# Optimization experiments

Measured on AMD Instinct MI355X. Metric: run time of the kernel, lower is better.

Reference implementation:

```python
import jax, jax.numpy as jnp
import numpy as np

N = 50000      # nodes
E = 800000     # unique directed edges (avg degree 16)
F = 64         # input_dim
D = 64         # output_dim (== F -> residual is identity)
ALPHA = 0.5
LCS_THR = 0.5  # enable_lcs_masking=True, lcs_threshold=0.5


def setup_inputs() -> dict:
    key = jax.random.key(0)
    ks = jax.random.split(key, 16)
    x = jax.random.normal(ks[0], (N, F), jnp.float32)
    src = jax.random.randint(ks[1], (E,), 0, N, jnp.int32)
    dst = jax.random.randint(ks[2], (E,), 0, N, jnp.int32)
    # integer-valued multiplicities in {1,2,3,4} (recurring-transaction counts)
    counts = jnp.floor(jax.random.uniform(ks[3], (E,), jnp.float32) * 4.0) + 1.0
    def lin(k, fan_in, shape):
        return jax.random.normal(k, shape, jnp.float32) / np.float32(np.sqrt(fan_in))
    return dict(
        x=x, counts=counts,
        W_s2d=lin(ks[4], F, (F, D)), b_s2d=jnp.zeros((D,), jnp.float32),
        W_d2s=lin(ks[5], F, (F, D)), b_d2s=jnp.zeros((D,), jnp.float32),
        W_l1=lin(ks[6], 2 * F, (2 * F, F)), b_l1=jnp.zeros((F,), jnp.float32),
        W_l2=lin(ks[7], F, (F, 1)), b_l2=jnp.zeros((1,), jnp.float32),
        W_g1=lin(ks[8], 2 * D, (2 * D, D)), b_g1=jnp.zeros((D,), jnp.float32),
        W_g2=lin(ks[9], D, (D, 1)), b_g2=jnp.zeros((1,), jnp.float32),
        src=src, dst=dst,
    )


def reference(x, counts, W_s2d, b_s2d, W_d2s, b_d2s,
              W_l1, b_l1, W_l2, b_l2, W_g1, b_g1, W_g2, b_g2,
              src, dst):
    # in/out degrees from full (unmasked) multiplicities, clamped at 1
    in_deg = jnp.maximum(jax.ops.segment_sum(counts, dst, num_segments=N), 1.0)
    out_deg = jnp.maximum(jax.ops.segment_sum(counts, src, num_segments=N), 1.0)

    # LCS per unique edge: sigmoid(MLP([x_src, x_dst])), detached in torch
    lcs_in = jnp.concatenate([x[src], x[dst]], axis=-1)          # [E, 2F]
    lcs = jax.nn.sigmoid(
        jax.nn.relu(lcs_in @ W_l1 + b_l1) @ W_l2 + b_l2)[:, 0]   # [E]
    lcs = jax.lax.stop_gradient(lcs)
    keep = (lcs >= LCS_THR).astype(x.dtype)                      # LCS masking

    # symmetric-normalized edge weights with multiplicity counts
    w = counts * keep * jax.lax.rsqrt(out_deg[src] * in_deg[dst])  # [E]

    # direction-aware message passing (redundancy-eliminated, per unique edge)
    h_s2d = x @ W_s2d + b_s2d                                    # [N, D]
    h_d2s = x @ W_d2s + b_d2s                                    # [N, D]
    m_in = jax.ops.segment_sum(w[:, None] * h_s2d[src], dst, num_segments=N)
    m_out = jax.ops.segment_sum(w[:, None] * h_d2s[dst], src, num_segments=N)

    # node-wise gating over inbound vs outbound flows
    gate = jax.nn.sigmoid(
        jax.nn.relu(jnp.concatenate([m_in, m_out], axis=-1) @ W_g1 + b_g1)
        @ W_g2 + b_g2)                                           # [N, 1]

    # gated alpha-blend + identity residual (input_dim == output_dim)
    out = ALPHA * gate * m_in + (1.0 - ALPHA) * (1.0 - gate) * m_out + x
    return out
```

## Files before the change

### kernel.cpp

```cpp
#include <hip/hip_runtime.h>
#include <math.h>


typedef unsigned long long u64;

#define SLOTS 56

__device__ __forceinline__ float bflo(unsigned u) { return __uint_as_float(u << 16); }
__device__ __forceinline__ float bfhi(unsigned u) { return __uint_as_float(u & 0xffff0000u); }
__device__ __forceinline__ unsigned rne16(float f) {
    unsigned u = __float_as_uint(f);
    return (u + 0x7fffu + ((u >> 16) & 1u)) >> 16;
}

__global__ __launch_bounds__(256) void proj_zero_kernel(
    const float* __restrict__ x,
    const float* __restrict__ Wl1,  const float* __restrict__ bl1,
    const float* __restrict__ Ws2d, const float* __restrict__ bs2d,
    const float* __restrict__ Wd2s, const float* __restrict__ bd2s,
    const float* __restrict__ Wg1,  float* __restrict__ Wg1q,
    float* __restrict__ A, float* __restrict__ B,
    unsigned* __restrict__ Ah, unsigned* __restrict__ Bh,
    unsigned* __restrict__ HSh, unsigned* __restrict__ HDh,
    int4* __restrict__ zp4, int nz4, int PB, int N)
{
    if (blockIdx.x >= PB) {
        if (blockIdx.x == PB + 64) {
            for (int i = threadIdx.x; i < 8192; i += 256) {
                const int k = i >> 6, c = i & 63;
                Wg1q[((k >> 2) * 64 + c) * 4 + (k & 3)] = Wg1[i];
            }
            return;
        }
        const int t0 = (blockIdx.x - PB) * 256 + threadIdx.x;
        const int stride = 64 * 256;
        const int4 z = make_int4(0, 0, 0, 0);
        for (int i = t0; i < nz4; i += stride) zp4[i] = z;
        return;
    }
    __shared__ float xs[64][64];
    const int tid = threadIdx.x;
    const int n0  = blockIdx.x * 64;
    const int wv  = tid >> 6;
    const int cc  = tid & 63;

    const float* Wbase; const float* bias; float* obase; unsigned* obh;
    switch (wv) {
        case 0:  Wbase = Wl1;           bias = bl1;     obase = A;       obh = Ah;  break;
        case 1:  Wbase = Wl1 + 64 * 64; bias = nullptr; obase = B;       obh = Bh;  break;
        case 2:  Wbase = Ws2d;          bias = bs2d;    obase = nullptr; obh = HSh; break;
        default: Wbase = Wd2s;          bias = bd2s;    obase = nullptr; obh = HDh; break;
    }

    float wr[64];
#pragma unroll
    for (int k = 0; k < 64; ++k) wr[k] = Wbase[k * 64 + cc];
    const float bv = bias ? bias[cc] : 0.f;

#pragma unroll
    for (int j = 0; j < 4; ++j) {
        int f4  = tid + j * 256;
        int row = f4 >> 4;
        int c4  = f4 & 15;
        int gn  = n0 + row;
        float4 v = (gn < N) ? ((const float4*)x)[(long)gn * 16 + c4]
                            : make_float4(0.f, 0.f, 0.f, 0.f);
        ((float4*)&xs[row][0])[c4] = v;
    }
    __syncthreads();

    const int nmax = (N - n0 < 64) ? (N - n0) : 64;
    for (int n = 0; n < nmax; ++n) {
        float acc = bv;
#pragma unroll
        for (int k = 0; k < 64; k += 4) {
            float4 xv = *((const float4*)&xs[n][k]);
            acc += xv.x * wr[k] + xv.y * wr[k + 1] + xv.z * wr[k + 2] + xv.w * wr[k + 3];
        }
        if (obase) obase[(long)(n0 + n) * 64 + cc] = acc;
        const float part = __shfl_xor(acc, 1);
        if ((cc & 1) == 0)
            obh[(long)(n0 + n) * 32 + (cc >> 1)] = (rne16(part) << 16) | rne16(acc);
    }
}

#define LCS_MARGIN 0.04f
__global__ __launch_bounds__(256) void edge_w_kernel(
    const int* __restrict__ src, const int* __restrict__ dst,
    const float* __restrict__ counts,
    const float* __restrict__ A, const float* __restrict__ B,
    const unsigned* __restrict__ Ah, const unsigned* __restrict__ Bh,
    const float* __restrict__ Wl2, const float* __restrict__ bl2,
    u64* __restrict__ pk, unsigned* __restrict__ rec, int N, int E)
{
    const int tid = threadIdx.x;
    const int e   = blockIdx.x * 32 + (tid >> 3);
    const int c   = tid & 7;
    if (e >= E) return;

    const int s = src[e];
    const int d = dst[e];
    const uint4  ua  = *((const uint4*)(Ah + (long)s * 32 + c * 4));
    const uint4  ub  = *((const uint4*)(Bh + (long)d * 32 + c * 4));
    const float4 wl0 = *((const float4*)(Wl2 + c * 8));
    const float4 wl1 = *((const float4*)(Wl2 + c * 8 + 4));

    float p = fmaxf(bflo(ua.x) + bflo(ub.x), 0.f) * wl0.x
            + fmaxf(bfhi(ua.x) + bfhi(ub.x), 0.f) * wl0.y
            + fmaxf(bflo(ua.y) + bflo(ub.y), 0.f) * wl0.z
            + fmaxf(bfhi(ua.y) + bfhi(ub.y), 0.f) * wl0.w
            + fmaxf(bflo(ua.z) + bflo(ub.z), 0.f) * wl1.x
            + fmaxf(bfhi(ua.z) + bfhi(ub.z), 0.f) * wl1.y
            + fmaxf(bflo(ua.w) + bflo(ub.w), 0.f) * wl1.z
            + fmaxf(bfhi(ua.w) + bfhi(ub.w), 0.f) * wl1.w;
    p += __shfl_xor(p, 1); p += __shfl_xor(p, 2); p += __shfl_xor(p, 4);

    float z = p + bl2[0];
    if (fabsf(z) < LCS_MARGIN) {
        const float4 a0 = *((const float4*)(A + (long)s * 64 + c * 8));
        const float4 a1 = *((const float4*)(A + (long)s * 64 + c * 8 + 4));
        const float4 b0 = *((const float4*)(B + (long)d * 64 + c * 8));
        const float4 b1 = *((const float4*)(B + (long)d * 64 + c * 8 + 4));
        float q = fmaxf(a0.x + b0.x, 0.f) * wl0.x + fmaxf(a0.y + b0.y, 0.f) * wl0.y
                + fmaxf(a0.z + b0.z, 0.f) * wl0.z + fmaxf(a0.w + b0.w, 0.f) * wl0.w
                + fmaxf(a1.x + b1.x, 0.f) * wl1.x + fmaxf(a1.y + b1.y, 0.f) * wl1.y
                + fmaxf(a1.z + b1.z, 0.f) * wl1.z + fmaxf(a1.w + b1.w, 0.f) * wl1.w;
        q += __shfl_xor(q, 1); q += __shfl_xor(q, 2); q += __shfl_xor(q, 4);
        z = q + bl2[0];
    }

    if (c == 0) {
        const u64 keep = (z >= 0.f) ? 1ull : 0ull;
        const unsigned ic = (unsigned)__float2int_rn(counts[e]);
        const u64 od = atomicAdd(pk + d,     (keep << 32) | (u64)ic);
        const u64 os = atomicAdd(pk + N + s, (keep << 32) | (u64)ic);
        if (keep) {
            rec[(long)d * SLOTS + (int)(od >> 32)]       = ((unsigned)s << 16) | ic;
            rec[(long)(N + s) * SLOTS + (int)(os >> 32)] = ((unsigned)d << 16) | ic;
        }
    }
}

__global__ __launch_bounds__(256) void gather_gate_kernel(
    const u64* __restrict__ pk, const unsigned* __restrict__ rec,
    const unsigned* __restrict__ HSh, const unsigned* __restrict__ HDh,
    const float* __restrict__ x,
    const float* __restrict__ Wg1q, const float* __restrict__ bg1,
    const float* __restrict__ Wg2, const float* __restrict__ bg2,
    float* __restrict__ out, int N)
{
    __shared__ float mbuf[4][128];
    const int tid  = threadIdx.x;
    const int wv   = tid >> 6;
    const int lane = tid & 63;
    const int g    = lane >> 3;
    const int c    = lane & 7;
    const int n    = blockIdx.x * 4 + wv;
    if (n >= N) return;

    const unsigned* pklo = (const unsigned*)pk;

    const u64 pin  = pk[n];
    const u64 pout = pk[N + n];
    const int ei = (int)(pin >> 32);
    const int eo = (int)(pout >> 32);
    const float qin  = 1.f / sqrtf(fmaxf((float)(unsigned)pin,  1.f));
    const float qout = 1.f / sqrtf(fmaxf((float)(unsigned)pout, 1.f));
    const unsigned* rin  = rec + (long)n * SLOTS;
    const unsigned* rout = rec + (long)(N + n) * SLOTS;

    float mi[8], mo[8];
#pragma unroll
    for (int j = 0; j < 8; ++j) { mi[j] = 0.f; mo[j] = 0.f; }

    int ii = g, jo = g;
    while ((ii < ei) || (jo < eo)) {
        const bool pa = ii < ei;
        const bool pb = jo < eo;
        const unsigned ra = rin[pa ? ii : 0];
        const unsigned rb = rout[pb ? jo : 0];
        const unsigned sa = ra >> 16;
        const unsigned sb = rb >> 16;
        const float dga = (float)pklo[2 * (N + (int)sa)];
        const float dgb = (float)pklo[2 * (int)sb];
        const float wa = pa ? (float)(ra & 0xFFu) * (1.f / sqrtf(fmaxf(dga, 1.f))) : 0.f;
        const float wb = pb ? (float)(rb & 0xFFu) * (1.f / sqrtf(fmaxf(dgb, 1.f))) : 0.f;
        const uint4 ua = *((const uint4*)(HSh + (long)sa * 32 + c * 4));
        const uint4 ub = *((const uint4*)(HDh + (long)sb * 32 + c * 4));
        mi[0] += wa * bflo(ua.x);  mo[0] += wb * bflo(ub.x);
        mi[1] += wa * bfhi(ua.x);  mo[1] += wb * bfhi(ub.x);
        mi[2] += wa * bflo(ua.y);  mo[2] += wb * bflo(ub.y);
        mi[3] += wa * bfhi(ua.y);  mo[3] += wb * bfhi(ub.y);
        mi[4] += wa * bflo(ua.z);  mo[4] += wb * bflo(ub.z);
        mi[5] += wa * bfhi(ua.z);  mo[5] += wb * bfhi(ub.z);
        mi[6] += wa * bflo(ua.w);  mo[6] += wb * bflo(ub.w);
        mi[7] += wa * bfhi(ua.w);  mo[7] += wb * bfhi(ub.w);
        ii += 8; jo += 8;
    }

#pragma unroll
    for (int j = 0; j < 8; ++j) {
        mi[j] += __shfl_xor(mi[j], 8);
        mi[j] += __shfl_xor(mi[j], 16);
        mi[j] += __shfl_xor(mi[j], 32);
        mo[j] += __shfl_xor(mo[j], 8);
        mo[j] += __shfl_xor(mo[j], 16);
        mo[j] += __shfl_xor(mo[j], 32);
    }
    if (g == 0) {
#pragma unroll
        for (int j = 0; j < 8; ++j) {
            mbuf[wv][c * 8 + j]      = mi[j] * qin;
            mbuf[wv][64 + c * 8 + j] = mo[j] * qout;
        }
    }

    float acc = bg1[lane];
    const float* mb = &mbuf[wv][0];
#pragma unroll 8
    for (int k4 = 0; k4 < 32; ++k4) {
        const float4 m4 = ((const float4*)mb)[k4];
        const float4 w4 = ((const float4*)Wg1q)[k4 * 64 + lane];
        acc += m4.x * w4.x + m4.y * w4.y + m4.z * w4.z + m4.w * w4.w;
    }
    float v = fmaxf(acc, 0.f) * Wg2[lane];
    v += __shfl_xor(v, 1);  v += __shfl_xor(v, 2);  v += __shfl_xor(v, 4);
    v += __shfl_xor(v, 8);  v += __shfl_xor(v, 16); v += __shfl_xor(v, 32);

    const float gate = 1.f / (1.f + expf(-(v + bg2[0])));
    const float miv = mb[lane];
    const float mov = mb[64 + lane];
    out[(long)n * 64 + lane] = 0.5f * gate * miv + 0.5f * (1.f - gate) * mov
                             + x[(long)n * 64 + lane];
}

extern "C" void kernel_launch(void* const* d_in, const int* in_sizes, int n_in,
                              void* d_out, int out_size, void* d_ws, size_t ws_size,
                              hipStream_t stream) {
    const float* x      = (const float*)d_in[0];
    const float* counts = (const float*)d_in[1];
    const float* Ws2d   = (const float*)d_in[2];
    const float* bs2d   = (const float*)d_in[3];
    const float* Wd2s   = (const float*)d_in[4];
    const float* bd2s   = (const float*)d_in[5];
    const float* Wl1    = (const float*)d_in[6];
    const float* bl1    = (const float*)d_in[7];
    const float* Wl2    = (const float*)d_in[8];
    const float* bl2    = (const float*)d_in[9];
    const float* Wg1    = (const float*)d_in[10];
    const float* bg1    = (const float*)d_in[11];
    const float* Wg2    = (const float*)d_in[12];
    const float* bg2    = (const float*)d_in[13];
    const int*   src    = (const int*)d_in[14];
    const int*   dst    = (const int*)d_in[15];

    const int N  = in_sizes[0] / 64;
    const int E  = in_sizes[14];
    const int PB = (N + 63) / 64;

    float* ws      = (float*)d_ws;
    float* Wg1q    = ws;
    float* A       = ws + 8192;
    float* B       = A + 64L * N;
    unsigned* Ah   = (unsigned*)(B + 64L * N);
    unsigned* Bh   = Ah + 32L * N;
    unsigned* HSh  = Bh + 32L * N;
    unsigned* HDh  = HSh + 32L * N;
    u64* pk        = (u64*)(HDh + 32L * N);
    unsigned* rec  = (unsigned*)(pk + 2L * N);

    proj_zero_kernel<<<PB + 65, 256, 0, stream>>>(
        x, Wl1, bl1, Ws2d, bs2d, Wd2s, bd2s, Wg1, Wg1q,
        A, B, Ah, Bh, HSh, HDh, (int4*)pk, N, PB, N);

    edge_w_kernel<<<(E + 31) / 32, 256, 0, stream>>>(
        src, dst, counts, A, B, Ah, Bh, Wl2, bl2, pk, rec, N, E);

    gather_gate_kernel<<<(N + 3) / 4, 256, 0, stream>>>(
        pk, rec, HSh, HDh, x, Wg1q, bg1, Wg2, bg2, (float*)d_out, N);
}
```

Baseline: 278.3 us.

## Register-block projection and gate kernels over multiple outputs per wave

New measurement: 280.1 us. Within noise of the previous version (+0.6%).

```diff
diff --git a/kernel.cpp b/kernel.cpp
--- a/kernel.cpp
+++ b/kernel.cpp
@@ -13,7 +13,7 @@
     return (u + 0x7fffu + ((u >> 16) & 1u)) >> 16;
 }
 
-__global__ __launch_bounds__(256) void proj_zero_kernel(
+__global__ __launch_bounds__(256, 2) void proj_zero_kernel(
     const float* __restrict__ x,
     const float* __restrict__ Wl1,  const float* __restrict__ bl1,
     const float* __restrict__ Ws2d, const float* __restrict__ bs2d,
@@ -39,23 +39,27 @@
         return;
     }
     __shared__ float xs[64][64];
-    const int tid = threadIdx.x;
-    const int n0  = blockIdx.x * 64;
-    const int wv  = tid >> 6;
-    const int cc  = tid & 63;
-
-    const float* Wbase; const float* bias; float* obase; unsigned* obh;
-    switch (wv) {
-        case 0:  Wbase = Wl1;           bias = bl1;     obase = A;       obh = Ah;  break;
-        case 1:  Wbase = Wl1 + 64 * 64; bias = nullptr; obase = B;       obh = Bh;  break;
-        case 2:  Wbase = Ws2d;          bias = bs2d;    obase = nullptr; obh = HSh; break;
-        default: Wbase = Wd2s;          bias = bd2s;    obase = nullptr; obh = HDh; break;
-    }
-
-    float wr[64];
-#pragma unroll
-    for (int k = 0; k < 64; ++k) wr[k] = Wbase[k * 64 + cc];
-    const float bv = bias ? bias[cc] : 0.f;
+    const int tid  = threadIdx.x;
+    const int n0   = blockIdx.x * 64;
+    const int wv   = tid >> 6;
+    const int cc   = tid & 63;
+    const int side = wv & 1;
+    const int par  = wv >> 1;
+
+    const float* W0 = side ? (Wl1 + 64 * 64) : Wl1;
+    const float* W1 = side ? Wd2s : Ws2d;
+    const float  b0 = side ? 0.f : bl1[cc];
+    const float  b1 = side ? bd2s[cc] : bs2d[cc];
+    float*    oA  = side ? B  : A;
+    unsigned* oAh = side ? Bh : Ah;
+    unsigned* oH  = side ? HDh : HSh;
+
+    float w0[64], w1[64];
+#pragma unroll
+    for (int k = 0; k < 64; ++k) {
+        w0[k] = W0[k * 64 + cc];
+        w1[k] = W1[k * 64 + cc];
+    }
 
 #pragma unroll
     for (int j = 0; j < 4; ++j) {
@@ -70,17 +74,22 @@
     __syncthreads();
 
     const int nmax = (N - n0 < 64) ? (N - n0) : 64;
-    for (int n = 0; n < nmax; ++n) {
-        float acc = bv;
+    for (int n = par; n < nmax; n += 2) {
+        float a0 = b0, a1 = b1;
 #pragma unroll
         for (int k = 0; k < 64; k += 4) {
             float4 xv = *((const float4*)&xs[n][k]);
-            acc += xv.x * wr[k] + xv.y * wr[k + 1] + xv.z * wr[k + 2] + xv.w * wr[k + 3];
-        }
-        if (obase) obase[(long)(n0 + n) * 64 + cc] = acc;
-        const float part = __shfl_xor(acc, 1);
-        if ((cc & 1) == 0)
-            obh[(long)(n0 + n) * 32 + (cc >> 1)] = (rne16(part) << 16) | rne16(acc);
+            a0 += xv.x * w0[k] + xv.y * w0[k + 1] + xv.z * w0[k + 2] + xv.w * w0[k + 3];
+            a1 += xv.x * w1[k] + xv.y * w1[k + 1] + xv.z * w1[k + 2] + xv.w * w1[k + 3];
+        }
+        const long gn = n0 + n;
+        oA[gn * 64 + cc] = a0;
+        const float p0 = __shfl_xor(a0, 1);
+        const float p1 = __shfl_xor(a1, 1);
+        if ((cc & 1) == 0) {
+            oAh[gn * 32 + (cc >> 1)] = (rne16(p0) << 16) | rne16(a0);
+            oH [gn * 32 + (cc >> 1)] = (rne16(p1) << 16) | rne16(a1);
+        }
     }
 }
 
@@ -149,89 +158,132 @@
     const float* __restrict__ Wg2, const float* __restrict__ bg2,
     float* __restrict__ out, int N)
 {
-    __shared__ float mbuf[4][128];
+    __shared__ float mbuf[16][128];
     const int tid  = threadIdx.x;
     const int wv   = tid >> 6;
     const int lane = tid & 63;
     const int g    = lane >> 3;
     const int c    = lane & 7;
-    const int n    = blockIdx.x * 4 + wv;
-    if (n >= N) return;
+    const int nb   = blockIdx.x * 16 + wv * 4;
 
     const unsigned* pklo = (const unsigned*)pk;
 
-    const u64 pin  = pk[n];
-    const u64 pout = pk[N + n];
-    const int ei = (int)(pin >> 32);
-    const int eo = (int)(pout >> 32);
-    const float qin  = 1.f / sqrtf(fmaxf((float)(unsigned)pin,  1.f));
-    const float qout = 1.f / sqrtf(fmaxf((float)(unsigned)pout, 1.f));
-    const unsigned* rin  = rec + (long)n * SLOTS;
-    const unsigned* rout = rec + (long)(N + n) * SLOTS;
-
-    float mi[8], mo[8];
-#pragma unroll
-    for (int j = 0; j < 8; ++j) { mi[j] = 0.f; mo[j] = 0.f; }
-
-    int ii = g, jo = g;
-    while ((ii < ei) || (jo < eo)) {
-        const bool pa = ii < ei;
-        const bool pb = jo < eo;
-        const unsigned ra = rin[pa ? ii : 0];
-        const unsigned rb = rout[pb ? jo : 0];
-        const unsigned sa = ra >> 16;
-        const unsigned sb = rb >> 16;
-        const float dga = (float)pklo[2 * (N + (int)sa)];
-        const float dgb = (float)pklo[2 * (int)sb];
-        const float wa = pa ? (float)(ra & 0xFFu) * (1.f / sqrtf(fmaxf(dga, 1.f))) : 0.f;
-        const float wb = pb ? (float)(rb & 0xFFu) * (1.f / sqrtf(fmaxf(dgb, 1.f))) : 0.f;
-        const uint4 ua = *((const uint4*)(HSh + (long)sa * 32 + c * 4));
-        const uint4 ub = *((const uint4*)(HDh + (long)sb * 32 + c * 4));
-        mi[0] += wa * bflo(ua.x);  mo[0] += wb * bflo(ub.x);
-        mi[1] += wa * bfhi(ua.x);  mo[1] += wb * bfhi(ub.x);
-        mi[2] += wa * bflo(ua.y);  mo[2] += wb * bflo(ub.y);
-        mi[3] += wa * bfhi(ua.y);  mo[3] += wb * bfhi(ub.y);
-        mi[4] += wa * bflo(ua.z);  mo[4] += wb * bflo(ub.z);
-        mi[5] += wa * bfhi(ua.z);  mo[5] += wb * bfhi(ub.z);
-        mi[6] += wa * bflo(ua.w);  mo[6] += wb * bflo(ub.w);
-        mi[7] += wa * bfhi(ua.w);  mo[7] += wb * bfhi(ub.w);
-        ii += 8; jo += 8;
-    }
-
-#pragma unroll
-    for (int j = 0; j < 8; ++j) {
-        mi[j] += __shfl_xor(mi[j], 8);
-        mi[j] += __shfl_xor(mi[j], 16);
-        mi[j] += __shfl_xor(mi[j], 32);
-        mo[j] += __shfl_xor(mo[j], 8);
-        mo[j] += __shfl_xor(mo[j], 16);
-        mo[j] += __shfl_xor(mo[j], 32);
-    }
-    if (g == 0) {
-#pragma unroll
-        for (int j = 0; j < 8; ++j) {
-            mbuf[wv][c * 8 + j]      = mi[j] * qin;
-            mbuf[wv][64 + c * 8 + j] = mo[j] * qout;
-        }
-    }
-
-    float acc = bg1[lane];
-    const float* mb = &mbuf[wv][0];
-#pragma unroll 8
+    for (int j = 0; j < 4; ++j) {
+        const int n   = nb + j;
+        const int row = wv * 4 + j;
+        if (n >= N) {
+            if (g == 0) {
+#pragma unroll
+                for (int q = 0; q < 8; ++q) {
+                    mbuf[row][c * 8 + q]      = 0.f;
+                    mbuf[row][64 + c * 8 + q] = 0.f;
+                }
+            }
+            continue;
+        }
+
+        const u64 pin  = pk[n];
+        const u64 pout = pk[N + n];
+        const int ei = (int)(pin >> 32);
+        const int eo = (int)(pout >> 32);
+        const float qin  = 1.f / sqrtf(fmaxf((float)(unsigned)pin,  1.f));
+        const float qout = 1.f / sqrtf(fmaxf((float)(unsigned)pout, 1.f));
+        const unsigned* rin  = rec + (long)n * SLOTS;
+        const unsigned* rout = rec + (long)(N + n) * SLOTS;
+
+        float mi[8], mo[8];
+#pragma unroll
+        for (int q = 0; q < 8; ++q) { mi[q] = 0.f; mo[q] = 0.f; }
+
+        int ii = g, jo = g;
+        while ((ii < ei) || (jo < eo)) {
+            const bool pa = ii < ei;
+            const bool pb = jo < eo;
+            const unsigned ra = rin[pa ? ii : 0];
+            const unsigned rb = rout[pb ? jo : 0];
+            const unsigned sa = ra >> 16;
+            const unsigned sb = rb >> 16;
+            const float dga = (float)pklo[2 * (N + (int)sa)];
+            const float dgb = (float)pklo[2 * (int)sb];
+            const float wa = pa ? (float)(ra & 0xFFu) * (1.f / sqrtf(fmaxf(dga, 1.f))) : 0.f;
+            const float wb = pb ? (float)(rb & 0xFFu) * (1.f / sqrtf(fmaxf(dgb, 1.f))) : 0.f;
+            const uint4 ua = *((const uint4*)(HSh + (long)sa * 32 + c * 4));
+            const uint4 ub = *((const uint4*)(HDh + (long)sb * 32 + c * 4));
+            mi[0] += wa * bflo(ua.x);  mo[0] += wb * bflo(ub.x);
+            mi[1] += wa * bfhi(ua.x);  mo[1] += wb * bfhi(ub.x);
+            mi[2] += wa * bflo(ua.y);  mo[2] += wb * bflo(ub.y);
+            mi[3] += wa * bfhi(ua.y);  mo[3] += wb * bfhi(ub.y);
+            mi[4] += wa * bflo(ua.z);  mo[4] += wb * bflo(ub.z);
+            mi[5] += wa * bfhi(ua.z);  mo[5] += wb * bfhi(ub.z);
+            mi[6] += wa * bflo(ua.w);  mo[6] += wb * bflo(ub.w);
+            mi[7] += wa * bfhi(ua.w);  mo[7] += wb * bfhi(ub.w);
+            ii += 8; jo += 8;
+        }
+
+#pragma unroll
+        for (int q = 0; q < 8; ++q) {
+            mi[q] += __shfl_xor(mi[q], 8);
+            mi[q] += __shfl_xor(mi[q], 16);
+            mi[q] += __shfl_xor(mi[q], 32);
+            mo[q] += __shfl_xor(mo[q], 8);
+            mo[q] += __shfl_xor(mo[q], 16);
+            mo[q] += __shfl_xor(mo[q], 32);
+        }
+        if (g == 0) {
+#pragma unroll
+            for (int q = 0; q < 8; ++q) {
+                mbuf[row][c * 8 + q]      = mi[q] * qin;
+                mbuf[row][64 + c * 8 + q] = mo[q] * qout;
+            }
+        }
+    }
+
+    const float bgv = bg1[lane];
+    float ac0 = bgv, ac1 = bgv, ac2 = bgv, ac3 = bgv;
+    const float* m0 = &mbuf[wv * 4 + 0][0];
+    const float* m1 = &mbuf[wv * 4 + 1][0];
+    const float* m2 = &mbuf[wv * 4 + 2][0];
+    const float* m3 = &mbuf[wv * 4 + 3][0];
+#pragma unroll 4
     for (int k4 = 0; k4 < 32; ++k4) {
-        const float4 m4 = ((const float4*)mb)[k4];
         const float4 w4 = ((const float4*)Wg1q)[k4 * 64 + lane];
-        acc += m4.x * w4.x + m4.y * w4.y + m4.z * w4.z + m4.w * w4.w;
-    }
-    float v = fmaxf(acc, 0.f) * Wg2[lane];
-    v += __shfl_xor(v, 1);  v += __shfl_xor(v, 2);  v += __shfl_xor(v, 4);
-    v += __shfl_xor(v, 8);  v += __shfl_xor(v, 16); v += __shfl_xor(v, 32);
-
-    const float gate = 1.f / (1.f + expf(-(v + bg2[0])));
-    const float miv = mb[lane];
-    const float mov = mb[64 + lane];
-    out[(long)n * 64 + lane] = 0.5f * gate * miv + 0.5f * (1.f - gate) * mov
-                             + x[(long)n * 64 + lane];
+        const float4 q0 = ((const float4*)m0)[k4];
+        const float4 q1 = ((const float4*)m1)[k4];
+        const float4 q2 = ((const float4*)m2)[k4];
+        const float4 q3 = ((const float4*)m3)[k4];
+        ac0 += q0.x * w4.x + q0.y * w4.y + q0.z * w4.z + q0.w * w4.w;
+        ac1 += q1.x * w4.x + q1.y * w4.y + q1.z * w4.z + q1.w * w4.w;
+        ac2 += q2.x * w4.x + q2.y * w4.y + q2.z * w4.z + q2.w * w4.w;
+        ac3 += q3.x * w4.x + q3.y * w4.y + q3.z * w4.z + q3.w * w4.w;
+    }
+    const float wg2 = Wg2[lane];
+    float v0 = fmaxf(ac0, 0.f) * wg2;
+    float v1 = fmaxf(ac1, 0.f) * wg2;
+    float v2 = fmaxf(ac2, 0.f) * wg2;
+    float v3 = fmaxf(ac3, 0.f) * wg2;
+#pragma unroll
+    for (int m = 1; m <= 32; m <<= 1) {
+        v0 += __shfl_xor(v0, m);
+        v1 += __shfl_xor(v1, m);
+        v2 += __shfl_xor(v2, m);
+        v3 += __shfl_xor(v3, m);
+    }
+    const float bb = bg2[0];
+    float gt[4];
+    gt[0] = 1.f / (1.f + expf(-(v0 + bb)));
+    gt[1] = 1.f / (1.f + expf(-(v1 + bb)));
+    gt[2] = 1.f / (1.f + expf(-(v2 + bb)));
+    gt[3] = 1.f / (1.f + expf(-(v3 + bb)));
+
+#pragma unroll
+    for (int j = 0; j < 4; ++j) {
+        const int n = nb + j;
+        if (n >= N) continue;
+        const float miv = mbuf[wv * 4 + j][lane];
+        const float mov = mbuf[wv * 4 + j][64 + lane];
+        out[(long)n * 64 + lane] = 0.5f * gt[j] * miv + 0.5f * (1.f - gt[j]) * mov
+                                 + x[(long)n * 64 + lane];
+    }
 }
 
 extern "C" void kernel_launch(void* const* d_in, const int* in_sizes, int n_in,
@@ -276,6 +328,6 @@
     edge_w_kernel<<<(E + 31) / 32, 256, 0, stream>>>(
         src, dst, counts, A, B, Ah, Bh, Wl2, bl2, pk, rec, N, E);
 
-    gather_gate_kernel<<<(N + 3) / 4, 256, 0, stream>>>(
+    gather_gate_kernel<<<(N + 15) / 16, 256, 0, stream>>>(
         pk, rec, HSh, HDh, x, Wg1q, bg1, Wg2, bg2, (float*)d_out, N);
 }
```
